# Performance work log

Hardware: AMD Instinct MI355X
Metric: run time of the kernel (lower is better)

Reference implementation:

```python
import jax, jax.numpy as jnp
import numpy as np

B, T, IO = 64, 1024, 1
H = 512
DELAY = 1


def _lstm_cell(x_t, h, c, Wih, Whh, bih, bhh):
    # PyTorch LSTMCell: gates = x@Wih.T + bih + h@Whh.T + bhh, gate order i,f,g,o
    gates = x_t @ Wih.T + bih + h @ Whh.T + bhh  # [B, 4H]
    i, f, g, o = jnp.split(gates, 4, axis=-1)
    i = jax.nn.sigmoid(i)
    f = jax.nn.sigmoid(f)
    g = jnp.tanh(g)
    o = jax.nn.sigmoid(o)
    c_new = f * c + i * g
    h_new = o * jnp.tanh(c_new)
    return h_new, c_new


def setup_inputs() -> dict:
    key = jax.random.key(0)
    ks = jax.random.split(key, 14)
    s = 0.02
    inp = {
        "x": jax.random.normal(ks[0], (B, T, IO), dtype=jnp.float32),
        # layer 0: input IO -> H
        "Wih0": jax.random.normal(ks[1], (4 * H, IO), dtype=jnp.float32) * s,
        "Whh0": jax.random.normal(ks[2], (4 * H, H), dtype=jnp.float32) * s,
        "bih0": jax.random.normal(ks[3], (4 * H,), dtype=jnp.float32) * s,
        "bhh0": jax.random.normal(ks[4], (4 * H,), dtype=jnp.float32) * s,
        # layer 1: H -> H
        "Wih1": jax.random.normal(ks[5], (4 * H, H), dtype=jnp.float32) * s,
        "Whh1": jax.random.normal(ks[6], (4 * H, H), dtype=jnp.float32) * s,
        "bih1": jax.random.normal(ks[7], (4 * H,), dtype=jnp.float32) * s,
        "bhh1": jax.random.normal(ks[8], (4 * H,), dtype=jnp.float32) * s,
        # layer 2: H -> H
        "Wih2": jax.random.normal(ks[9], (4 * H, H), dtype=jnp.float32) * s,
        "Whh2": jax.random.normal(ks[10], (4 * H, H), dtype=jnp.float32) * s,
        "bih2": jax.random.normal(ks[11], (4 * H,), dtype=jnp.float32) * s,
        "bhh2": jax.random.normal(ks[12], (4 * H,), dtype=jnp.float32) * s,
        # output head: H -> IO
        "Wout": jax.random.normal(ks[13], (IO, H), dtype=jnp.float32) * s,
        "bout": jnp.zeros((IO,), dtype=jnp.float32),
    }
    return inp


def reference(x, Wih0, Whh0, bih0, bhh0, Wih1, Whh1, bih1, bhh1,
              Wih2, Whh2, bih2, bhh2, Wout, bout):
    # delay: shift input right by DELAY steps, zero-pad front
    pad = jnp.zeros_like(x[:, :DELAY, :])
    x = jnp.concatenate([pad, x[:, :-DELAY, :]], axis=1)

    h0 = jnp.zeros((x.shape[0], H), dtype=x.dtype)
    carry0 = (h0, h0, h0, h0, h0, h0)  # (h0,c0,h1,c1,h2,c2)

    xs = jnp.swapaxes(x, 0, 1)  # [T, B, IO]

    def step(carry, x_t):
        h0, c0, h1, c1, h2, c2 = carry
        h0, c0 = _lstm_cell(x_t, h0, c0, Wih0, Whh0, bih0, bhh0)
        h1, c1 = _lstm_cell(h0, h1, c1, Wih1, Whh1, bih1, bhh1)
        h2, c2 = _lstm_cell(h1, h2, c2, Wih2, Whh2, bih2, bhh2)
        o_t = h2 @ Wout.T + bout  # [B, IO]
        return (h0, c0, h1, c1, h2, c2), o_t

    _, outs = jax.lax.scan(step, carry0, xs)  # [T, B, IO]
    return jnp.swapaxes(outs, 0, 1)  # [B, T, IO]
```

## Files before the change

kernel.cpp:

```cpp
#include <hip/hip_runtime.h>
#include <stdint.h>

#define Hdim 512
#define Bsz 64
#define Tlen 1024
#define RING 8
#define GR (RING * 16 * Hdim)
#define FSTR 16
#define LROW 516

typedef __attribute__((ext_vector_type(8))) short short8;
typedef __attribute__((ext_vector_type(4))) short bf16x4;
typedef __attribute__((ext_vector_type(4))) float f32x4;
typedef unsigned long long u64;
struct u64x2 { u64 lo, hi; };

__device__ __forceinline__ short f2bf(float f) {
  uint32_t u = __float_as_uint(f);
  u += 0x7fffu + ((u >> 16) & 1u);
  return (short)(u >> 16);
}

__device__ __forceinline__ f32x4 mfma16(short8 a, short8 b, f32x4 c) {
  return __builtin_amdgcn_mfma_f32_16x16x32_bf16(a, b, c, 0, 0, 0);
}

__device__ __forceinline__ void vm_wait0() {
  asm volatile("s_waitcnt vmcnt(0)" ::: "memory");
  __builtin_amdgcn_sched_barrier(0);
}

__device__ __forceinline__ void wait_multi(const uint32_t* pp, uint32_t tgt) {
  uint32_t it = 0;
  for (;;) {
    uint32_t v = __hip_atomic_load(pp, __ATOMIC_RELAXED, __HIP_MEMORY_SCOPE_AGENT);
    if (__all((int)(v >= tgt))) break;
    __builtin_amdgcn_s_sleep(1);
    if (++it > (1u << 20)) break;
  }
}

__device__ __forceinline__ void stage_slot(const short* __restrict__ src,
                                           short* __restrict__ lds,
                                           int wave, int lane) {
#pragma unroll
  for (int j = 0; j < 4; ++j) {
    int r = wave * 4 + j;
    const u64* s = (const u64*)(src + r * 512);
    u64* dst = (u64*)(lds + r * LROW);
    u64 v0 = __hip_atomic_load(s + lane,      __ATOMIC_RELAXED, __HIP_MEMORY_SCOPE_AGENT);
    u64 v1 = __hip_atomic_load(s + lane + 64, __ATOMIC_RELAXED, __HIP_MEMORY_SCOPE_AGENT);
    dst[lane]      = v0;
    dst[lane + 64] = v1;
  }
}

__device__ __forceinline__ short8 frag_read(const short* __restrict__ lds,
                                            int lane, int ks) {
  int base = (lane & 15) * LROW + (lane >> 4) * 8 + ks * 32;
  bf16x4 lo = *(const bf16x4*)(lds + base);
  bf16x4 hi = *(const bf16x4*)(lds + base + 4);
  short8 r;
  r[0] = lo[0]; r[1] = lo[1]; r[2] = lo[2]; r[3] = lo[3];
  r[4] = hi[0]; r[5] = hi[1]; r[6] = hi[2]; r[7] = hi[3];
  return r;
}

__global__ void out_init(float* out, const float* bout) {
  int i = blockIdx.x * 256 + threadIdx.x;
  if (i < Bsz * Tlen) out[i] = bout[0];
}

__global__ void pack_kernel(const float* __restrict__ Whh0,
                            const float* __restrict__ Wih1, const float* __restrict__ Whh1,
                            const float* __restrict__ Wih2, const float* __restrict__ Whh2,
                            short* __restrict__ Bpack) {
  int ch = blockIdx.x * 256 + threadIdx.x;
  const int L0C = 64 * 16 * 2 * 64;
  const int L12C = 64 * 32 * 2 * 64;
  if (ch >= L0C + 2 * L12C) return;
  int layer, rel, KS;
  const float* Wih;
  const float* Whh;
  if (ch < L0C) { layer = 0; rel = ch; KS = 16; Wih = nullptr; Whh = Whh0; }
  else if (ch < L0C + L12C) { layer = 1; rel = ch - L0C; KS = 32; Wih = Wih1; Whh = Whh1; }
  else { layer = 2; rel = ch - L0C - L12C; KS = 32; Wih = Wih2; Whh = Whh2; }
  int lane = rel & 63;
  int nt = (rel >> 6) & 1;
  int rest = rel >> 7;
  int ks = rest % KS;
  int dw = rest / KS;
  int w = dw & 3;
  int d = dw >> 2;
  int col = nt * 16 + (lane & 15);
  int row = (col >> 3) * Hdim + d * 32 + w * 8 + (col & 7);
  int kbase = ks * 32 + (lane >> 4) * 8;
  short8 v;
#pragma unroll
  for (int e = 0; e < 8; ++e) {
    int k = kbase + e;
    float wt;
    if (layer == 0) wt = Whh[row * Hdim + k];
    else wt = (k < Hdim) ? Wih[row * Hdim + k] : Whh[row * Hdim + (k - Hdim)];
    v[e] = f2bf(wt);
  }
  ((short8*)Bpack)[ch] = v;
}

__global__ __launch_bounds__(256, 1)
void lstm_persist(const float* __restrict__ x,
                  const float* __restrict__ Wih0v,
                  const float* __restrict__ bih0, const float* __restrict__ bhh0,
                  const float* __restrict__ bih1, const float* __restrict__ bhh1,
                  const float* __restrict__ bih2, const float* __restrict__ bhh2,
                  const float* __restrict__ Wout,
                  const short* __restrict__ Bpack,
                  short* __restrict__ rings,
                  uint32_t* __restrict__ flags,
                  float* __restrict__ out) {
  const int blk = blockIdx.x;
  const int layer = blk >> 6;
  const int g = (blk >> 4) & 3;
  const int d = blk & 15;
  const int tid = threadIdx.x;
  const int lane = tid & 63;
  const int wave = tid >> 6;

  __shared__ short ldsA[16 * LROW];
  __shared__ short ldsB[16 * LROW];
  __shared__ short hbuf[16][32];
  __shared__ float pbuf[4][16];

  short8 bw[32][2];
  {
    const short8* bp = (const short8*)Bpack;
    if (layer == 0) {
#pragma unroll
      for (int ks = 0; ks < 16; ++ks) {
        bw[ks][0] = bp[((((d * 4 + wave) * 16 + ks) * 2 + 0) * 64) + lane];
        bw[ks][1] = bp[((((d * 4 + wave) * 16 + ks) * 2 + 1) * 64) + lane];
        asm volatile("" : "+v"(bw[ks][0]), "+v"(bw[ks][1]));
      }
    } else {
      const int base = (layer == 1) ? 131072 : 393216;
#pragma unroll
      for (int ks = 0; ks < 32; ++ks) {
        bw[ks][0] = bp[base + (((d * 4 + wave) * 32 + ks) * 2 + 0) * 64 + lane];
        bw[ks][1] = bp[base + (((d * 4 + wave) * 32 + ks) * 2 + 1) * 64 + lane];
        asm volatile("" : "+v"(bw[ks][0]), "+v"(bw[ks][1]));
      }
    }
  }

  const float* bih = (layer == 0) ? bih0 : (layer == 1 ? bih1 : bih2);
  const float* bhh = (layer == 0) ? bhh0 : (layer == 1 ? bhh1 : bhh2);
  const int dimb = d * 32 + wave * 8 + (lane & 7);
  const int row0 = (((lane & 15) >> 3)) * Hdim + dimb;
  const int row1 = (((lane & 15) >> 3) + 2) * Hdim + dimb;
  const float bias0 = bih[row0] + bhh[row0];
  const float bias1 = bih[row1] + bhh[row1];
  float xw0 = 0.f, xw1 = 0.f, woutd = 0.f;
  if (layer == 0) { xw0 = Wih0v[row0]; xw1 = Wih0v[row1]; }
  if (layer == 2) woutd = Wout[dimb];

  uint32_t* flagsO = flags + ((layer * 4 + g) * 16) * FSTR;
  const uint32_t* flagsP = flags + (((layer - 1) * 4 + g) * 16) * FSTR;
  const uint32_t* flagsN = flags + (((layer + 1) * 4 + g) * 16) * FSTR;
  short* ringLG = rings + (layer * 4 + g) * GR;
  const short* ringPG = rings + ((layer - 1) * 4 + g) * GR;

  const uint32_t* p1ptr = (layer > 0 && lane < 16) ? flagsP + lane * FSTR : flagsO;
  const uint32_t* p2ptr = (lane < 16) ? flagsO + lane * FSTR
                        : (lane < 32 && layer < 2) ? flagsN + (lane - 16) * FSTR : flagsO;
  const bool p2bp = (lane >= 16 && lane < 32 && layer < 2);

  const int bR = 4 * (lane >> 4);

  float c[4] = {0.f, 0.f, 0.f, 0.f};

  for (int t = 0; t < Tlen; ++t) {
    f32x4 acc0 = {bias0, bias0, bias0, bias0};
    f32x4 acc1 = {bias1, bias1, bias1, bias1};
    if (layer > 0) {
      if (wave == 0) {
        uint32_t tgt1 = (lane < 16) ? (uint32_t)(t + 1) : 0u;
        wait_multi(p1ptr, tgt1);
      }
      __syncthreads();
      stage_slot(ringPG + (t & (RING - 1)) * (16 * Hdim), ldsA, wave, lane);
      __syncthreads();
#pragma unroll
      for (int ks = 0; ks < 16; ++ks) {
        short8 a = frag_read(ldsA, lane, ks);
        acc0 = mfma16(a, bw[ks][0], acc0);
        acc1 = mfma16(a, bw[ks][1], acc1);
      }
    } else if (t > 0) {
#pragma unroll
      for (int r = 0; r < 4; ++r) {
        float xv = x[(g * 16 + bR + r) * Tlen + (t - 1)];
        acc0[r] += xw0 * xv;
        acc1[r] += xw1 * xv;
      }
    }

    if (wave == 0) {
      uint32_t tgt2;
      if (lane < 16) tgt2 = (uint32_t)t;
      else if (p2bp) tgt2 = (t + 1 >= RING) ? (uint32_t)(t + 1 - RING) : 0u;
      else tgt2 = 0u;
      wait_multi(p2ptr, tgt2);
    }
    __syncthreads();

    if (t > 0) {
      stage_slot(ringLG + ((t - 1) & (RING - 1)) * (16 * Hdim), ldsB, wave, lane);
      __syncthreads();
      if (layer == 0) {
#pragma unroll
        for (int ks = 0; ks < 16; ++ks) {
          short8 a = frag_read(ldsB, lane, ks);
          acc0 = mfma16(a, bw[ks][0], acc0);
          acc1 = mfma16(a, bw[ks][1], acc1);
        }
      } else {
#pragma unroll
        for (int ks = 0; ks < 16; ++ks) {
          short8 a = frag_read(ldsB, lane, ks);
          acc0 = mfma16(a, bw[16 + ks][0], acc0);
          acc1 = mfma16(a, bw[16 + ks][1], acc1);
        }
      }
    }

    float parts[4];
#pragma unroll
    for (int r = 0; r < 4; ++r) {
      float a0 = acc0[r], a1 = acc1[r];
      float p0 = __shfl_xor(a0, 8);
      float p1 = __shfl_xor(a1, 8);
      float iv = 1.f / (1.f + __expf(-a0));
      float fv = 1.f / (1.f + __expf(-p0));
      float gv = tanhf(a1);
      float ov = 1.f / (1.f + __expf(-p1));
      c[r] = fv * c[r] + iv * gv;
      float hv = ov * tanhf(c[r]);
      if ((lane & 8) == 0) hbuf[bR + r][wave * 8 + (lane & 7)] = f2bf(hv);
      parts[r] = hv * woutd;
    }
    if (layer == 2) {
#pragma unroll
      for (int r = 0; r < 4; ++r) {
        parts[r] += __shfl_xor(parts[r], 1);
        parts[r] += __shfl_xor(parts[r], 2);
        parts[r] += __shfl_xor(parts[r], 4);
        if ((lane & 15) == 0) pbuf[wave][bR + r] = parts[r];
      }
    }

    __syncthreads();
    if (wave == 0) {
      short* hout = ringLG + (t & (RING - 1)) * (16 * Hdim);
      int row = lane >> 2, q = lane & 3;
      u64x2 u;
      u.lo = ((const u64*)&hbuf[row][q * 8])[0];
      u.hi = ((const u64*)&hbuf[row][q * 8])[1];
      u64* dst = (u64*)(hout + row * Hdim + d * 32 + q * 8);
      __hip_atomic_store(dst,     u.lo, __ATOMIC_RELAXED, __HIP_MEMORY_SCOPE_AGENT);
      __hip_atomic_store(dst + 1, u.hi, __ATOMIC_RELAXED, __HIP_MEMORY_SCOPE_AGENT);
      vm_wait0();
      if (lane == 0)
        __hip_atomic_store(flagsO + d * FSTR, (uint32_t)(t + 1), __ATOMIC_RELAXED,
                           __HIP_MEMORY_SCOPE_AGENT);
      if (layer == 2 && lane < 16) {
        float s = pbuf[0][lane] + pbuf[1][lane] + pbuf[2][lane] + pbuf[3][lane];
        atomicAdd(out + (g * 16 + lane) * Tlen + t, s);
      }
    }
  }
}

extern "C" void kernel_launch(void* const* d_in, const int* in_sizes, int n_in,
                              void* d_out, int out_size, void* d_ws, size_t ws_size,
                              hipStream_t stream) {
  const float* x    = (const float*)d_in[0];
  const float* Wih0 = (const float*)d_in[1];
  const float* Whh0 = (const float*)d_in[2];
  const float* bih0 = (const float*)d_in[3];
  const float* bhh0 = (const float*)d_in[4];
  const float* Wih1 = (const float*)d_in[5];
  const float* Whh1 = (const float*)d_in[6];
  const float* bih1 = (const float*)d_in[7];
  const float* bhh1 = (const float*)d_in[8];
  const float* Wih2 = (const float*)d_in[9];
  const float* Whh2 = (const float*)d_in[10];
  const float* bih2 = (const float*)d_in[11];
  const float* bhh2 = (const float*)d_in[12];
  const float* Wout = (const float*)d_in[13];
  const float* bout = (const float*)d_in[14];

  char* ws = (char*)d_ws;
  short* Bpack    = (short*)ws;
  short* rings    = (short*)(ws + 10485760);
  uint32_t* flags = (uint32_t*)(ws + 12058624);
  float* out      = (float*)d_out;

  (void)hipMemsetAsync(flags, 0, 12 * 16 * FSTR * sizeof(uint32_t), stream);
  out_init<<<(Bsz * Tlen + 255) / 256, 256, 0, stream>>>(out, bout);
  pack_kernel<<<2560, 256, 0, stream>>>(Whh0, Wih1, Whh1, Wih2, Whh2, Bpack);
  lstm_persist<<<192, 256, 0, stream>>>(x, Wih0, bih0, bhh0, bih1, bhh1, bih2, bhh2,
                                        Wout, Bpack, rings, flags, out);
}
```

Measured before the change: 5.846 ms.

## Merge per-step flag waits and batch both ring loads before one barrier

Combines the two separate cross-block flag waits (previous layer input and own-layer recurrence) into a single wait_multi call covering all dependencies. Then it issues all global loads for both ring slots before writing them to LDS, so only one barrier pair is needed per step. The h-state publish is also spread over two waves instead of one. This removes one wait/barrier round-trip per timestep and overlaps the two loads' latency. The cost is that the recurrent MFMA on the input slot can no longer start before the own-layer flag is ready, and the extra barrier before the flag store adds some sync.

```diff
diff --git a/kernel.cpp b/kernel.cpp
--- a/kernel.cpp
+++ b/kernel.cpp
@@ -37,21 +37,6 @@
     if (__all((int)(v >= tgt))) break;
     __builtin_amdgcn_s_sleep(1);
     if (++it > (1u << 20)) break;
-  }
-}
-
-__device__ __forceinline__ void stage_slot(const short* __restrict__ src,
-                                           short* __restrict__ lds,
-                                           int wave, int lane) {
-#pragma unroll
-  for (int j = 0; j < 4; ++j) {
-    int r = wave * 4 + j;
-    const u64* s = (const u64*)(src + r * 512);
-    u64* dst = (u64*)(lds + r * LROW);
-    u64 v0 = __hip_atomic_load(s + lane,      __ATOMIC_RELAXED, __HIP_MEMORY_SCOPE_AGENT);
-    u64 v1 = __hip_atomic_load(s + lane + 64, __ATOMIC_RELAXED, __HIP_MEMORY_SCOPE_AGENT);
-    dst[lane]      = v0;
-    dst[lane + 64] = v1;
   }
 }
 
@@ -169,26 +154,72 @@
   short* ringLG = rings + (layer * 4 + g) * GR;
   const short* ringPG = rings + ((layer - 1) * 4 + g) * GR;
 
-  const uint32_t* p1ptr = (layer > 0 && lane < 16) ? flagsP + lane * FSTR : flagsO;
-  const uint32_t* p2ptr = (lane < 16) ? flagsO + lane * FSTR
-                        : (lane < 32 && layer < 2) ? flagsN + (lane - 16) * FSTR : flagsO;
-  const bool p2bp = (lane >= 16 && lane < 32 && layer < 2);
+  const uint32_t* pptr;
+  int pmode;
+  if (lane < 16) { pptr = flagsO + lane * FSTR; pmode = 0; }
+  else if (lane < 32 && layer > 0) { pptr = flagsP + (lane - 16) * FSTR; pmode = 1; }
+  else if (lane >= 32 && lane < 48 && layer < 2) { pptr = flagsN + (lane - 32) * FSTR; pmode = 2; }
+  else { pptr = flagsO; pmode = 3; }
 
   const int bR = 4 * (lane >> 4);
 
   float c[4] = {0.f, 0.f, 0.f, 0.f};
 
   for (int t = 0; t < Tlen; ++t) {
+    if (wave == 0) {
+      uint32_t tgt;
+      if (pmode == 0) tgt = (uint32_t)t;
+      else if (pmode == 1) tgt = (uint32_t)(t + 1);
+      else if (pmode == 2) tgt = (t + 1 >= RING) ? (uint32_t)(t + 1 - RING) : 0u;
+      else tgt = 0u;
+      wait_multi(pptr, tgt);
+    }
+    __syncthreads();
+
+    {
+      const bool doA = (layer > 0);
+      const bool doB = (t > 0);
+      u64 va[8], vb[8];
+      if (doA) {
+        const short* srcA = ringPG + (t & (RING - 1)) * (16 * Hdim);
+#pragma unroll
+        for (int j = 0; j < 4; ++j) {
+          const u64* s = (const u64*)(srcA + (wave * 4 + j) * 512);
+          va[2 * j]     = __hip_atomic_load(s + lane,      __ATOMIC_RELAXED, __HIP_MEMORY_SCOPE_AGENT);
+          va[2 * j + 1] = __hip_atomic_load(s + lane + 64, __ATOMIC_RELAXED, __HIP_MEMORY_SCOPE_AGENT);
+        }
+      }
+      if (doB) {
+        const short* srcB = ringLG + ((t - 1) & (RING - 1)) * (16 * Hdim);
+#pragma unroll
+        for (int j = 0; j < 4; ++j) {
+          const u64* s = (const u64*)(srcB + (wave * 4 + j) * 512);
+          vb[2 * j]     = __hip_atomic_load(s + lane,      __ATOMIC_RELAXED, __HIP_MEMORY_SCOPE_AGENT);
+          vb[2 * j + 1] = __hip_atomic_load(s + lane + 64, __ATOMIC_RELAXED, __HIP_MEMORY_SCOPE_AGENT);
+        }
+      }
+      if (doA) {
+#pragma unroll
+        for (int j = 0; j < 4; ++j) {
+          u64* dst = (u64*)(ldsA + (wave * 4 + j) * LROW);
+          dst[lane]      = va[2 * j];
+          dst[lane + 64] = va[2 * j + 1];
+        }
+      }
+      if (doB) {
+#pragma unroll
+        for (int j = 0; j < 4; ++j) {
+          u64* dst = (u64*)(ldsB + (wave * 4 + j) * LROW);
+          dst[lane]      = vb[2 * j];
+          dst[lane + 64] = vb[2 * j + 1];
+        }
+      }
+    }
+    __syncthreads();
+
     f32x4 acc0 = {bias0, bias0, bias0, bias0};
     f32x4 acc1 = {bias1, bias1, bias1, bias1};
     if (layer > 0) {
-      if (wave == 0) {
-        uint32_t tgt1 = (lane < 16) ? (uint32_t)(t + 1) : 0u;
-        wait_multi(p1ptr, tgt1);
-      }
-      __syncthreads();
-      stage_slot(ringPG + (t & (RING - 1)) * (16 * Hdim), ldsA, wave, lane);
-      __syncthreads();
 #pragma unroll
       for (int ks = 0; ks < 16; ++ks) {
         short8 a = frag_read(ldsA, lane, ks);
@@ -203,19 +234,7 @@
         acc1[r] += xw1 * xv;
       }
     }
-
-    if (wave == 0) {
-      uint32_t tgt2;
-      if (lane < 16) tgt2 = (uint32_t)t;
-      else if (p2bp) tgt2 = (t + 1 >= RING) ? (uint32_t)(t + 1 - RING) : 0u;
-      else tgt2 = 0u;
-      wait_multi(p2ptr, tgt2);
-    }
-    __syncthreads();
-
     if (t > 0) {
-      stage_slot(ringLG + ((t - 1) & (RING - 1)) * (16 * Hdim), ldsB, wave, lane);
-      __syncthreads();
       if (layer == 0) {
 #pragma unroll
         for (int ks = 0; ks < 16; ++ks) {
@@ -259,20 +278,20 @@
     }
 
     __syncthreads();
-    if (wave == 0) {
+    {
       short* hout = ringLG + (t & (RING - 1)) * (16 * Hdim);
-      int row = lane >> 2, q = lane & 3;
-      u64x2 u;
-      u.lo = ((const u64*)&hbuf[row][q * 8])[0];
-      u.hi = ((const u64*)&hbuf[row][q * 8])[1];
-      u64* dst = (u64*)(hout + row * Hdim + d * 32 + q * 8);
-      __hip_atomic_store(dst,     u.lo, __ATOMIC_RELAXED, __HIP_MEMORY_SCOPE_AGENT);
-      __hip_atomic_store(dst + 1, u.hi, __ATOMIC_RELAXED, __HIP_MEMORY_SCOPE_AGENT);
+      if (tid < 128) {
+        int row = tid >> 3, cch = tid & 7;
+        u64 v = ((const u64*)&hbuf[row][0])[cch];
+        u64* dst = (u64*)(hout + row * Hdim + d * 32) + cch;
+        __hip_atomic_store(dst, v, __ATOMIC_RELAXED, __HIP_MEMORY_SCOPE_AGENT);
+      }
       vm_wait0();
-      if (lane == 0)
+      __syncthreads();
+      if (tid == 0)
         __hip_atomic_store(flagsO + d * FSTR, (uint32_t)(t + 1), __ATOMIC_RELAXED,
                            __HIP_MEMORY_SCOPE_AGENT);
-      if (layer == 2 && lane < 16) {
+      if (layer == 2 && wave == 0 && lane < 16) {
         float s = pbuf[0][lane] + pbuf[1][lane] + pbuf[2][lane] + pbuf[3][lane];
         atomicAdd(out + (g * 16 + lane) * Tlen + t, s);
       }
```

New measurement: 5.163 ms. 1.13x faster.

## Embed step tags in ring data packets to replace separate flag polling

Applied to the files above, without the earlier changes.

Each 16-byte ring packet now holds a timestep tag followed by six bf16 hidden values. Consumers poll the data directly with coherent dwordx4 loads and check the tags, so the separate flag wait, barrier and staging round trip per step are gone. A separate progress counter is kept only for ring-slot backpressure, and the wide LDS fragment read replaces two half reads. The cost is more memory traffic (tag overhead, a larger ring, a bigger memset), plus the assumption that each 16-byte store becomes visible atomically.

```diff
diff --git a/kernel.cpp b/kernel.cpp
--- a/kernel.cpp
+++ b/kernel.cpp
@@ -5,15 +5,13 @@
 #define Bsz 64
 #define Tlen 1024
 #define RING 8
-#define GR (RING * 16 * Hdim)
 #define FSTR 16
-#define LROW 516
+#define LROW 520
+#define SLOTS 12288
 
 typedef __attribute__((ext_vector_type(8))) short short8;
-typedef __attribute__((ext_vector_type(4))) short bf16x4;
+typedef __attribute__((ext_vector_type(4))) int i32x4;
 typedef __attribute__((ext_vector_type(4))) float f32x4;
-typedef unsigned long long u64;
-struct u64x2 { u64 lo, hi; };
 
 __device__ __forceinline__ short f2bf(float f) {
   uint32_t u = __float_as_uint(f);
@@ -25,45 +23,95 @@
   return __builtin_amdgcn_mfma_f32_16x16x32_bf16(a, b, c, 0, 0, 0);
 }
 
-__device__ __forceinline__ void vm_wait0() {
-  asm volatile("s_waitcnt vmcnt(0)" ::: "memory");
-  __builtin_amdgcn_sched_barrier(0);
-}
-
-__device__ __forceinline__ void wait_multi(const uint32_t* pp, uint32_t tgt) {
+__device__ __forceinline__ void poll6(const short* b, uint32_t tag, i32x4* o) {
+  const short* p0 = b;       const short* p1 = b + 8;
+  const short* p2 = b + 16;  const short* p3 = b + 24;
+  const short* p4 = b + 32;  const short* p5 = b + 40;
   uint32_t it = 0;
   for (;;) {
-    uint32_t v = __hip_atomic_load(pp, __ATOMIC_RELAXED, __HIP_MEMORY_SCOPE_AGENT);
-    if (__all((int)(v >= tgt))) break;
+    i32x4 r0, r1, r2, r3, r4, r5;
+    asm volatile(
+        "global_load_dwordx4 %0, %6, off sc0 sc1\n\t"
+        "global_load_dwordx4 %1, %7, off sc0 sc1\n\t"
+        "global_load_dwordx4 %2, %8, off sc0 sc1\n\t"
+        "global_load_dwordx4 %3, %9, off sc0 sc1\n\t"
+        "global_load_dwordx4 %4, %10, off sc0 sc1\n\t"
+        "global_load_dwordx4 %5, %11, off sc0 sc1\n\t"
+        "s_waitcnt vmcnt(0)"
+        : "=&v"(r0), "=&v"(r1), "=&v"(r2), "=&v"(r3), "=&v"(r4), "=&v"(r5)
+        : "v"(p0), "v"(p1), "v"(p2), "v"(p3), "v"(p4), "v"(p5)
+        : "memory");
+    bool ok = ((uint32_t)r0[0] == tag) && ((uint32_t)r1[0] == tag) &&
+              ((uint32_t)r2[0] == tag) && ((uint32_t)r3[0] == tag) &&
+              ((uint32_t)r4[0] == tag) && ((uint32_t)r5[0] == tag);
+    if (ok || ++it > (1u << 15)) {
+      o[0] = r0; o[1] = r1; o[2] = r2; o[3] = r3; o[4] = r4; o[5] = r5;
+      return;
+    }
     __builtin_amdgcn_s_sleep(1);
-    if (++it > (1u << 20)) break;
-  }
-}
-
-__device__ __forceinline__ void stage_slot(const short* __restrict__ src,
-                                           short* __restrict__ lds,
-                                           int wave, int lane) {
-#pragma unroll
-  for (int j = 0; j < 4; ++j) {
-    int r = wave * 4 + j;
-    const u64* s = (const u64*)(src + r * 512);
-    u64* dst = (u64*)(lds + r * LROW);
-    u64 v0 = __hip_atomic_load(s + lane,      __ATOMIC_RELAXED, __HIP_MEMORY_SCOPE_AGENT);
-    u64 v1 = __hip_atomic_load(s + lane + 64, __ATOMIC_RELAXED, __HIP_MEMORY_SCOPE_AGENT);
-    dst[lane]      = v0;
-    dst[lane + 64] = v1;
-  }
+  }
+}
+
+__device__ __forceinline__ void poll12(const short* a, uint32_t ta,
+                                       const short* b, uint32_t tb,
+                                       i32x4* oa, i32x4* ob) {
+  const short* a0 = a;       const short* a1 = a + 8;
+  const short* a2 = a + 16;  const short* a3 = a + 24;
+  const short* a4 = a + 32;  const short* a5 = a + 40;
+  const short* b0 = b;       const short* b1 = b + 8;
+  const short* b2 = b + 16;  const short* b3 = b + 24;
+  const short* b4 = b + 32;  const short* b5 = b + 40;
+  uint32_t it = 0;
+  for (;;) {
+    i32x4 r0, r1, r2, r3, r4, r5, r6, r7, r8, r9, r10, r11;
+    asm volatile(
+        "global_load_dwordx4 %0, %12, off sc0 sc1\n\t"
+        "global_load_dwordx4 %1, %13, off sc0 sc1\n\t"
+        "global_load_dwordx4 %2, %14, off sc0 sc1\n\t"
+        "global_load_dwordx4 %3, %15, off sc0 sc1\n\t"
+        "global_load_dwordx4 %4, %16, off sc0 sc1\n\t"
+        "global_load_dwordx4 %5, %17, off sc0 sc1\n\t"
+        "global_load_dwordx4 %6, %18, off sc0 sc1\n\t"
+        "global_load_dwordx4 %7, %19, off sc0 sc1\n\t"
+        "global_load_dwordx4 %8, %20, off sc0 sc1\n\t"
+        "global_load_dwordx4 %9, %21, off sc0 sc1\n\t"
+        "global_load_dwordx4 %10, %22, off sc0 sc1\n\t"
+        "global_load_dwordx4 %11, %23, off sc0 sc1\n\t"
+        "s_waitcnt vmcnt(0)"
+        : "=&v"(r0), "=&v"(r1), "=&v"(r2), "=&v"(r3), "=&v"(r4), "=&v"(r5),
+          "=&v"(r6), "=&v"(r7), "=&v"(r8), "=&v"(r9), "=&v"(r10), "=&v"(r11)
+        : "v"(a0), "v"(a1), "v"(a2), "v"(a3), "v"(a4), "v"(a5),
+          "v"(b0), "v"(b1), "v"(b2), "v"(b3), "v"(b4), "v"(b5)
+        : "memory");
+    bool ok = ((uint32_t)r0[0] == ta) && ((uint32_t)r1[0] == ta) &&
+              ((uint32_t)r2[0] == ta) && ((uint32_t)r3[0] == ta) &&
+              ((uint32_t)r4[0] == ta) && ((uint32_t)r5[0] == ta) &&
+              ((uint32_t)r6[0] == tb) && ((uint32_t)r7[0] == tb) &&
+              ((uint32_t)r8[0] == tb) && ((uint32_t)r9[0] == tb) &&
+              ((uint32_t)r10[0] == tb) && ((uint32_t)r11[0] == tb);
+    if (ok || ++it > (1u << 15)) {
+      oa[0] = r0; oa[1] = r1; oa[2] = r2; oa[3] = r3; oa[4] = r4; oa[5] = r5;
+      ob[0] = r6; ob[1] = r7; ob[2] = r8; ob[3] = r9; ob[4] = r10; ob[5] = r11;
+      return;
+    }
+    __builtin_amdgcn_s_sleep(1);
+  }
+}
+
+__device__ __forceinline__ void unpack6(const i32x4* c, short* ldsdst) {
+  uint32_t* dst = (uint32_t*)ldsdst;
+#pragma unroll
+  for (int j = 0; j < 5; ++j) {
+    dst[3 * j]     = (uint32_t)c[j][1];
+    dst[3 * j + 1] = (uint32_t)c[j][2];
+    dst[3 * j + 2] = (uint32_t)c[j][3];
+  }
+  dst[15] = (uint32_t)c[5][1];
 }
 
 __device__ __forceinline__ short8 frag_read(const short* __restrict__ lds,
                                             int lane, int ks) {
-  int base = (lane & 15) * LROW + (lane >> 4) * 8 + ks * 32;
-  bf16x4 lo = *(const bf16x4*)(lds + base);
-  bf16x4 hi = *(const bf16x4*)(lds + base + 4);
-  short8 r;
-  r[0] = lo[0]; r[1] = lo[1]; r[2] = lo[2]; r[3] = lo[3];
-  r[4] = hi[0]; r[5] = hi[1]; r[6] = hi[2]; r[7] = hi[3];
-  return r;
+  return *(const short8*)(lds + (lane & 15) * LROW + (lane >> 4) * 8 + ks * 32);
 }
 
 __global__ void out_init(float* out, const float* bout) {
@@ -115,13 +163,14 @@
                   const float* __restrict__ bih2, const float* __restrict__ bhh2,
                   const float* __restrict__ Wout,
                   const short* __restrict__ Bpack,
-                  short* __restrict__ rings,
-                  uint32_t* __restrict__ flags,
+                  short* __restrict__ ringT,
+                  uint32_t* __restrict__ prog,
                   float* __restrict__ out) {
   const int blk = blockIdx.x;
   const int layer = blk >> 6;
   const int g = (blk >> 4) & 3;
   const int d = blk & 15;
+  const int dom = layer * 4 + g;
   const int tid = threadIdx.x;
   const int lane = tid & 63;
   const int wave = tid >> 6;
@@ -163,32 +212,51 @@
   if (layer == 0) { xw0 = Wih0v[row0]; xw1 = Wih0v[row1]; }
   if (layer == 2) woutd = Wout[dimb];
 
-  uint32_t* flagsO = flags + ((layer * 4 + g) * 16) * FSTR;
-  const uint32_t* flagsP = flags + (((layer - 1) * 4 + g) * 16) * FSTR;
-  const uint32_t* flagsN = flags + (((layer + 1) * 4 + g) * 16) * FSTR;
-  short* ringLG = rings + (layer * 4 + g) * GR;
-  const short* ringPG = rings + ((layer - 1) * 4 + g) * GR;
-
-  const uint32_t* p1ptr = (layer > 0 && lane < 16) ? flagsP + lane * FSTR : flagsO;
-  const uint32_t* p2ptr = (lane < 16) ? flagsO + lane * FSTR
-                        : (lane < 32 && layer < 2) ? flagsN + (lane - 16) * FSTR : flagsO;
-  const bool p2bp = (lane >= 16 && lane < 32 && layer < 2);
+  const int prow = tid >> 4;
+  const int pblk = tid & 15;
+  short* myRing = ringT + (size_t)dom * 8 * SLOTS;
+  const short* pvRing = ringT + (size_t)(dom - 4) * 8 * SLOTS;
 
   const int bR = 4 * (lane >> 4);
-
   float c[4] = {0.f, 0.f, 0.f, 0.f};
 
+  const int qrow = tid / 6;
+  const int qj = tid - qrow * 6;
+
   for (int t = 0; t < Tlen; ++t) {
+    i32x4 ca[6], cb[6];
+    {
+      const short* ownp = myRing + (size_t)((t - 1) & 7) * SLOTS + (size_t)tid * 48;
+      const short* prvp = pvRing + (size_t)(t & 7) * SLOTS + (size_t)tid * 48;
+      if (layer > 0 && t > 0) poll12(prvp, (uint32_t)(t + 1), ownp, (uint32_t)t, ca, cb);
+      else if (layer > 0)     poll6(prvp, (uint32_t)(t + 1), ca);
+      else if (t > 0)         poll6(ownp, (uint32_t)t, cb);
+    }
+    if (tid >= 224 && t >= RING) {
+      int l32 = tid - 224;
+      const uint32_t* pf = nullptr;
+      uint32_t tg = 0;
+      if (l32 < 16) { pf = prog + (dom * 16 + l32) * FSTR; tg = (uint32_t)(t - 6); }
+      else if (layer < 2) { pf = prog + ((dom + 4) * 16 + (l32 - 16)) * FSTR; tg = (uint32_t)(t - 7); }
+      if (pf) {
+        uint32_t it = 0;
+        while (__hip_atomic_load(pf, __ATOMIC_RELAXED, __HIP_MEMORY_SCOPE_AGENT) < tg) {
+          __builtin_amdgcn_s_sleep(1);
+          if (++it > (1u << 15)) break;
+        }
+      }
+    }
+    if (layer > 0) unpack6(ca, ldsA + prow * LROW + pblk * 32);
+    if (t > 0)     unpack6(cb, ldsB + prow * LROW + pblk * 32);
+    __syncthreads();
+
+    if (tid == 0)
+      __hip_atomic_store(prog + (dom * 16 + d) * FSTR, (uint32_t)(t + 1),
+                         __ATOMIC_RELAXED, __HIP_MEMORY_SCOPE_AGENT);
+
     f32x4 acc0 = {bias0, bias0, bias0, bias0};
     f32x4 acc1 = {bias1, bias1, bias1, bias1};
     if (layer > 0) {
-      if (wave == 0) {
-        uint32_t tgt1 = (lane < 16) ? (uint32_t)(t + 1) : 0u;
-        wait_multi(p1ptr, tgt1);
-      }
-      __syncthreads();
-      stage_slot(ringPG + (t & (RING - 1)) * (16 * Hdim), ldsA, wave, lane);
-      __syncthreads();
 #pragma unroll
       for (int ks = 0; ks < 16; ++ks) {
         short8 a = frag_read(ldsA, lane, ks);
@@ -203,19 +271,7 @@
         acc1[r] += xw1 * xv;
       }
     }
-
-    if (wave == 0) {
-      uint32_t tgt2;
-      if (lane < 16) tgt2 = (uint32_t)t;
-      else if (p2bp) tgt2 = (t + 1 >= RING) ? (uint32_t)(t + 1 - RING) : 0u;
-      else tgt2 = 0u;
-      wait_multi(p2ptr, tgt2);
-    }
-    __syncthreads();
-
     if (t > 0) {
-      stage_slot(ringLG + ((t - 1) & (RING - 1)) * (16 * Hdim), ldsB, wave, lane);
-      __syncthreads();
       if (layer == 0) {
 #pragma unroll
         for (int ks = 0; ks < 16; ++ks) {
@@ -259,23 +315,25 @@
     }
 
     __syncthreads();
-    if (wave == 0) {
-      short* hout = ringLG + (t & (RING - 1)) * (16 * Hdim);
-      int row = lane >> 2, q = lane & 3;
-      u64x2 u;
-      u.lo = ((const u64*)&hbuf[row][q * 8])[0];
-      u.hi = ((const u64*)&hbuf[row][q * 8])[1];
-      u64* dst = (u64*)(hout + row * Hdim + d * 32 + q * 8);
-      __hip_atomic_store(dst,     u.lo, __ATOMIC_RELAXED, __HIP_MEMORY_SCOPE_AGENT);
-      __hip_atomic_store(dst + 1, u.hi, __ATOMIC_RELAXED, __HIP_MEMORY_SCOPE_AGENT);
-      vm_wait0();
-      if (lane == 0)
-        __hip_atomic_store(flagsO + d * FSTR, (uint32_t)(t + 1), __ATOMIC_RELAXED,
-                           __HIP_MEMORY_SCOPE_AGENT);
-      if (layer == 2 && lane < 16) {
-        float s = pbuf[0][lane] + pbuf[1][lane] + pbuf[2][lane] + pbuf[3][lane];
-        atomicAdd(out + (g * 16 + lane) * Tlen + t, s);
-      }
+
+    if (tid < 96) {
+      uint32_t h01 = *(const uint32_t*)&hbuf[qrow][6 * qj];
+      uint32_t h23 = 0, h45 = 0;
+      if (qj < 5) {
+        h23 = *(const uint32_t*)&hbuf[qrow][6 * qj + 2];
+        h45 = *(const uint32_t*)&hbuf[qrow][6 * qj + 4];
+      }
+      i32x4 v;
+      v[0] = (int)(t + 1); v[1] = (int)h01; v[2] = (int)h23; v[3] = (int)h45;
+      short* dst = myRing + (size_t)(t & 7) * SLOTS +
+                   (size_t)((qrow * 16 + d) * 6 + qj) * 8;
+      asm volatile("global_store_dwordx4 %0, %1, off sc0 sc1"
+                   :: "v"(dst), "v"(v) : "memory");
+    }
+    if (layer == 2 && tid >= 128 && tid < 144) {
+      int b = tid - 128;
+      float s = pbuf[0][b] + pbuf[1][b] + pbuf[2][b] + pbuf[3][b];
+      atomicAdd(out + (g * 16 + b) * Tlen + t, s);
     }
   }
 }
@@ -300,14 +358,14 @@
   const float* bout = (const float*)d_in[14];
 
   char* ws = (char*)d_ws;
-  short* Bpack    = (short*)ws;
-  short* rings    = (short*)(ws + 10485760);
-  uint32_t* flags = (uint32_t*)(ws + 12058624);
-  float* out      = (float*)d_out;
-
-  (void)hipMemsetAsync(flags, 0, 12 * 16 * FSTR * sizeof(uint32_t), stream);
+  short* Bpack   = (short*)ws;
+  short* ringT   = (short*)(ws + 10485760);
+  uint32_t* prog = (uint32_t*)(ws + 12845056);
+  float* out     = (float*)d_out;
+
+  (void)hipMemsetAsync(ringT, 0, 2359296 + 12288, stream);
   out_init<<<(Bsz * Tlen + 255) / 256, 256, 0, stream>>>(out, bout);
   pack_kernel<<<2560, 256, 0, stream>>>(Whh0, Wih1, Whh1, Wih2, Whh2, Bpack);
   lstm_persist<<<192, 256, 0, stream>>>(x, Wih0, bih0, bhh0, bih1, bhh1, bih2, bhh2,
-                                        Wout, Bpack, rings, flags, out);
-}
+                                        Wout, Bpack, ringT, prog, out);
+}
```

Measured after the change: 6.033 ms. 1.03x slower.
